# Optimization experiments

Measured on AMD Instinct MI355X. Metric: run time of the kernel, lower is better.

## Reference

```python
import jax, jax.numpy as jnp
import numpy as np

N, E, F, HID, HEADS, L, B, R = 50000, 400000, 64, 256, 4, 4, 16, 8
C = HID // HEADS  # per-head channels = 64
LN_EPS = 1e-5
NEG_SLOPE = 0.2  # GATConv LeakyReLU default


def _posenc(n, d):
    pos = jnp.arange(n, dtype=jnp.float32)[:, None]
    i = jnp.arange(d, dtype=jnp.float32)[None, :]
    rates = 1.0 / 10000.0 ** (2.0 * jnp.floor(i / 2.0) / d)
    ang = pos * rates
    return jnp.where(jnp.arange(d)[None, :] % 2 == 0, jnp.sin(ang), jnp.cos(ang))


def _layernorm(x, g, b):
    mu = x.mean(-1, keepdims=True)
    var = ((x - mu) ** 2).mean(-1, keepdims=True)
    return (x - mu) * jax.lax.rsqrt(var + LN_EPS) * g + b


def _gat_layer(x, src, dst, W, a_src, a_dst, bias):
    # x: [N, HID]; W: [HID, HID]; a_src/a_dst: [HEADS, C]; bias: [HID]
    h = (x @ W).reshape(N, HEADS, C)
    s_src = (h * a_src[None]).sum(-1)  # [N, HEADS]
    s_dst = (h * a_dst[None]).sum(-1)  # [N, HEADS]
    e = jax.nn.leaky_relu(s_src[src] + s_dst[dst], NEG_SLOPE)  # [E', HEADS]
    m = jax.ops.segment_max(e, dst, num_segments=N)
    ex = jnp.exp(e - m[dst])
    denom = jax.ops.segment_sum(ex, dst, num_segments=N)
    alpha = ex / denom[dst]  # softmax over incoming edges per dst node
    out = jax.ops.segment_sum(alpha[:, :, None] * h[src], dst, num_segments=N)
    return out.reshape(N, HID) + bias


def setup_inputs() -> dict:
    key = jax.random.key(0)
    ks = jax.random.split(key, 20)
    sc = 0.05
    batch = jnp.sort(jax.random.randint(ks[2], (N,), 0, B))
    return {
        "x": jax.random.normal(ks[0], (N, F), jnp.float32),
        "region_emb_w": jax.random.normal(ks[3], (R, F), jnp.float32) * sc,
        "in_proj_w": jax.random.normal(ks[4], (3 * F, HID), jnp.float32) * sc,
        "in_proj_b": jnp.zeros((HID,), jnp.float32),
        "gat_w": jax.random.normal(ks[5], (L, HID, HID), jnp.float32) * sc,
        "att_src": jax.random.normal(ks[6], (L, HEADS, C), jnp.float32) * sc,
        "att_dst": jax.random.normal(ks[7], (L, HEADS, C), jnp.float32) * sc,
        "gat_b": jnp.zeros((L, HID), jnp.float32),
        "ln_g": jnp.ones((L, HID), jnp.float32),
        "ln_b": jnp.zeros((L, HID), jnp.float32),
        "ro_w1": jax.random.normal(ks[8], (HID, HID), jnp.float32) * sc,
        "ro_b1": jnp.zeros((HID,), jnp.float32),
        "ro_w2": jax.random.normal(ks[9], (HID, HID), jnp.float32) * sc,
        "ro_b2": jnp.zeros((HID,), jnp.float32),
        "edge_index": jax.random.randint(ks[1], (2, E), 0, N),
        "batch": batch,
        "region_ids": jax.random.randint(ks[10], (N,), 0, R),
    }


def reference(x, region_emb_w, in_proj_w, in_proj_b, gat_w, att_src, att_dst,
              gat_b, ln_g, ln_b, ro_w1, ro_b1, ro_w2, ro_b2,
              edge_index, batch, region_ids):
    # input features: x | region embedding | sinusoidal posenc  -> [N, 3F]
    feats = jnp.concatenate([x, region_emb_w[region_ids], _posenc(N, F)], axis=-1)
    h = feats @ in_proj_w + in_proj_b
    # add self loops once (GATConv add_self_loops=True)
    loop = jnp.arange(N)
    src = jnp.concatenate([edge_index[0], loop])
    dst = jnp.concatenate([edge_index[1], loop])
    for l in range(L):
        h = _gat_layer(h, src, dst, gat_w[l], att_src[l], att_dst[l], gat_b[l])
        h = _layernorm(jax.nn.relu(h), ln_g[l], ln_b[l])
        # dropout is identity in eval mode
    # global mean pool over graphs
    sums = jax.ops.segment_sum(h, batch, num_segments=B)
    cnts = jax.ops.segment_sum(jnp.ones((N,), h.dtype), batch, num_segments=B)
    pooled = sums / jnp.maximum(cnts, 1.0)[:, None]  # [B, HID]
    out = jax.nn.gelu(pooled @ ro_w1 + ro_b1, approximate=False) @ ro_w2 + ro_b2
    return out
```

## Files before the change

kernel.cpp:

```cpp
#include <hip/hip_runtime.h>
#include <cmath>

typedef unsigned short u16;
typedef unsigned char u8;
typedef unsigned int u32;
typedef short bf16x8 __attribute__((ext_vector_type(8)));
typedef float f32x4 __attribute__((ext_vector_type(4)));
typedef float f32x2 __attribute__((ext_vector_type(2)));

#define NN 50000
#define MP 50048
#define EE 400000
#define ET 450000
#define HIDD 256
#define KIN 192
#define LN_EPSF 1e-5f

__device__ __forceinline__ float bf2f(u16 u){ return __uint_as_float(((u32)u)<<16); }
__device__ __forceinline__ u16 f2bf(float f){
  u32 x = __float_as_uint(f);
  u32 r = x + 0x7fffu + ((x>>16)&1u);
  return (u16)(r>>16);
}
__device__ __forceinline__ u32 pack2(float a, float b){ return (u32)f2bf(a) | ((u32)f2bf(b)<<16); }
__device__ __forceinline__ u8 f2fp8(float v){
  return (u8)(__builtin_amdgcn_cvt_pk_fp8_f32(v, v, 0, false) & 0xff);
}

__device__ __forceinline__ void dma16(const u16* g, u16* lds){
  __builtin_amdgcn_global_load_lds(
      (const __attribute__((address_space(1))) void*)g,
      (__attribute__((address_space(3))) void*)lds, 16, 0, 0);
}

__global__ __launch_bounds__(256) void k_setup(
    const float* __restrict__ x, const float* __restrict__ remb, const int* __restrict__ rid,
    u16* __restrict__ feats,
    const float* __restrict__ ipw, const float* __restrict__ gatw,
    u16* __restrict__ wtin, u16* __restrict__ wtl,
    const float* __restrict__ asrc, const float* __restrict__ adst, u16* __restrict__ vmat,
    const int* __restrict__ ei, int* __restrict__ deg)
{
  int b = blockIdx.x;
  if (b < 1564){
    int u = b*256 + threadIdx.x;
    int n = u >> 3;
    int c0 = (u & 7) * 8;
    uint4 o = {0u,0u,0u,0u};
    if (n < NN){
      const float* xp = x + (size_t)n*64 + c0;
      float4 v0 = *(const float4*)xp;
      float4 v1 = *(const float4*)(xp + 4);
      o.x = pack2(v0.x, v0.y); o.y = pack2(v0.z, v0.w);
      o.z = pack2(v1.x, v1.y); o.w = pack2(v1.z, v1.w);
    }
    *(uint4*)(feats + (size_t)n*192 + c0) = o;
  } else if (b < 3128){
    int u = (b-1564)*256 + threadIdx.x;
    int n = u >> 3;
    int c0 = (u & 7) * 8;
    uint4 o = {0u,0u,0u,0u};
    if (n < NN){
      const float* rp = remb + (size_t)rid[n]*64 + c0;
      float4 v0 = *(const float4*)rp;
      float4 v1 = *(const float4*)(rp + 4);
      o.x = pack2(v0.x, v0.y); o.y = pack2(v0.z, v0.w);
      o.z = pack2(v1.x, v1.y); o.w = pack2(v1.z, v1.w);
    }
    *(uint4*)(feats + (size_t)n*192 + 64 + c0) = o;
  } else if (b < 4692){
    int u = (b-3128)*256 + threadIdx.x;
    int n = u >> 3;
    int i0 = (u & 7) * 8;
    uint4 o = {0u,0u,0u,0u};
    if (n < NN){
      float fn = (float)n;
      float os[8];
      #pragma unroll
      for (int m=0;m<4;++m){
        float rate = exp2f(-(float)(i0 + 2*m) * (1.0f/64.0f) * 13.287712379549449f);
        float s, c;
        __sincosf(fn * rate, &s, &c);
        os[2*m] = s; os[2*m+1] = c;
      }
      o.x = pack2(os[0], os[1]); o.y = pack2(os[2], os[3]);
      o.z = pack2(os[4], os[5]); o.w = pack2(os[6], os[7]);
    }
    *(uint4*)(feats + (size_t)n*192 + 128 + i0) = o;
  } else if (b < 5908){
    int idx = (b - 4692)*256 + threadIdx.x;
    if (idx < 49152){
      int n = idx / 192, k = idx - n*192;
      wtin[idx] = f2bf(ipw[k*256 + n]);
    } else {
      int j = idx - 49152;
      if (j < 262144){
        int l = j >> 16, rem = j & 65535;
        int n = rem >> 8, k = rem & 255;
        wtl[j] = f2bf(gatw[l*65536 + k*256 + n]);
      }
    }
  } else if (b < 5972){
    int idx = (b - 5908)*256 + threadIdx.x;
    if (idx < 16384){
      int l = idx >> 12, rem = idx & 4095, v = rem >> 8, k = rem & 255;
      float s = 0.f;
      if (v < 8){
        const float* a = (v < 4) ? (asrc + l*256 + v*64) : (adst + l*256 + (v-4)*64);
        const float* w = gatw + (size_t)l*65536 + k*256 + (v & 3)*64;
        #pragma unroll 8
        for (int c=0;c<64;++c) s += w[c]*a[c];
      }
      vmat[idx] = f2bf(s);
    }
  } else {
    int i = (b - 5972)*256 + threadIdx.x;
    if (i < ET){
      int d = (i < EE) ? ei[EE + i] : (i - EE);
      atomicAdd(&deg[d], 1);
    }
  }
}

__global__ void k_scan1(const int* __restrict__ deg, int* __restrict__ row_off, int* __restrict__ part){
  __shared__ int s[256];
  int n = blockIdx.x*256 + threadIdx.x;
  int v = (n < NN) ? deg[n] : 0;
  s[threadIdx.x] = v;
  __syncthreads();
  for (int off=1; off<256; off<<=1){
    int t = (threadIdx.x >= off) ? s[threadIdx.x - off] : 0;
    __syncthreads();
    s[threadIdx.x] += t;
    __syncthreads();
  }
  if (n < NN) row_off[n] = s[threadIdx.x] - v;
  if (threadIdx.x == 255) part[blockIdx.x] = s[255];
}

__global__ void k_scan23(int* __restrict__ row_off, const int* __restrict__ part, int nparts){
  __shared__ int sp[256];
  int t = threadIdx.x;
  sp[t] = (t < nparts && t < (int)blockIdx.x) ? part[t] : 0;
  __syncthreads();
  for (int off=128; off; off>>=1){
    if (t < off) sp[t] += sp[t+off];
    __syncthreads();
  }
  int n = blockIdx.x*256 + t;
  if (n < NN) row_off[n] += sp[0];
}

__global__ void k_scatter(const int* __restrict__ ei, const int* __restrict__ row_off,
                          int* __restrict__ cur, int* __restrict__ csr_src){
  int i = blockIdx.x*blockDim.x + threadIdx.x;
  if (i >= ET) return;
  int s, d;
  if (i < EE){ s = ei[i]; d = ei[EE + i]; } else { s = i - EE; d = i - EE; }
  int pos = row_off[d] + atomicAdd(&cur[d], 1);
  csr_src[pos] = s;
}

template<int K>
__global__ __launch_bounds__(256, 3) void k_gemm(
    const u16* __restrict__ A, const u16* __restrict__ Wt,
    const float* __restrict__ bias, const u16* __restrict__ vmat,
    float* __restrict__ ss, float* __restrict__ sd,
    u16* __restrict__ C, u8* __restrict__ C8, int M)
{
  __shared__ u16 Asl[2][128*32];
  __shared__ u16 Bsl[2][128*32];
  int tid = threadIdx.x;
  int wave = tid >> 6, lane = tid & 63, quad = lane >> 4, lm = lane & 15;
  int r0 = blockIdx.x * 128;
  int cb = blockIdx.y;
  int rW = (wave >> 1) * 64;
  int cW = (wave & 1) * 64;
  bool doScore = vmat && (cb == 0) && ((wave & 1) == 0);

  f32x4 acc[4][4] = {};
  f32x4 accs[4] = {};

  auto stage = [&](int buf, int k0){
    for (int m = wave; m < 8; m += 4){
      int s = m*64 + lane;
      int r = s >> 2, p = s & 3;
      int c = p ^ ((r >> 2) & 3);
      dma16(A + (size_t)(r0 + r)*K + k0 + c*8, &Asl[buf][m*512]);
    }
    for (int m = wave; m < 8; m += 4){
      int s = m*64 + lane;
      int r = s >> 2, p = s & 3;
      int c = p ^ ((r >> 2) & 3);
      dma16(Wt + (size_t)(cb*128 + r)*K + k0 + c*8, &Bsl[buf][m*512]);
    }
  };

  stage(0, 0);
  __syncthreads();

  for (int ks = 0; ks < K/32; ++ks){
    int cur = ks & 1;
    if (ks + 1 < K/32) stage(cur ^ 1, (ks+1)*32);

    bf16x8 a[4], b[4];
    #pragma unroll
    for (int i=0;i<4;++i){
      int row = rW + i*16 + lm;
      int slot = row*4 + (quad ^ ((row >> 2) & 3));
      a[i] = *(const bf16x8*)(&Asl[cur][slot*8]);
    }
    #pragma unroll
    for (int j=0;j<4;++j){
      int row = cW + j*16 + lm;
      int slot = row*4 + (quad ^ ((row >> 2) & 3));
      b[j] = *(const bf16x8*)(&Bsl[cur][slot*8]);
    }
    #pragma unroll
    for (int i=0;i<4;++i)
      #pragma unroll
      for (int j=0;j<4;++j)
        acc[i][j] = __builtin_amdgcn_mfma_f32_16x16x32_bf16(a[i], b[j], acc[i][j], 0, 0, 0);
    if (doScore){
      bf16x8 bs = *(const bf16x8*)(vmat + (size_t)lm*K + ks*32 + quad*8);
      #pragma unroll
      for (int i=0;i<4;++i)
        accs[i] = __builtin_amdgcn_mfma_f32_16x16x32_bf16(a[i], bs, accs[i], 0, 0, 0);
    }
    __syncthreads();
  }

  if (doScore){
    #pragma unroll
    for (int i=0;i<4;++i){
      #pragma unroll
      for (int r=0;r<4;++r){
        int row = r0 + rW + i*16 + quad*4 + r;
        if (row < M){
          if (lm < 4)      ss[row*4 + lm]     = accs[i][r];
          else if (lm < 8) sd[row*4 + lm - 4] = accs[i][r];
        }
      }
    }
  }

  #pragma unroll
  for (int i=0;i<4;++i){
    #pragma unroll
    for (int r=0;r<4;++r){
      int row = r0 + rW + i*16 + quad*4 + r;
      if (row < M){
        #pragma unroll
        for (int j=0;j<4;++j){
          int col = cb*128 + cW + j*16 + lm;
          float v = acc[i][j][r];
          if (bias) v += bias[col];
          if (C)  C[(size_t)row*256 + col] = f2bf(v);
          if (C8) C8[(size_t)row*256 + col] = f2fp8(v);
        }
      }
    }
  }
}

__global__ __launch_bounds__(256) void k_aggregate(
    const u8* __restrict__ h8, const float* __restrict__ ssrc, const float* __restrict__ sdst,
    const int* __restrict__ row_off, const int* __restrict__ deg, const int* __restrict__ csr_src,
    const float* __restrict__ bias, const float* __restrict__ g, const float* __restrict__ bb,
    u16* __restrict__ hout, u8* __restrict__ hout8)
{
  int wv = (blockIdx.x*blockDim.x + threadIdx.x) >> 6;
  int lane = threadIdx.x & 63;
  int half = lane >> 5;
  int hl = lane & 31;
  int n = wv*2 + half;
  if (n >= NN) return;
  int c0 = hl*8;
  int head = hl >> 3;
  float sdh = sdst[n*4 + head];
  int ro = row_off[n];
  int dg = deg[n];
  float denA = 0.f, denB = 0.f;
  float a0=0,a1=0,a2=0,a3=0,a4=0,a5=0,a6=0,a7=0;
  float b0=0,b1=0,b2=0,b3=0,b4=0,b5=0,b6=0,b7=0;

  int sA = csr_src[ro];
  int sB = (1 < dg) ? csr_src[ro + 1] : 0;
  uint2 uA = *(const uint2*)(h8 + (size_t)sA*HIDD + c0);
  uint2 uB = *(const uint2*)(h8 + (size_t)sB*HIDD + c0);
  float fA = ssrc[sA*4 + head];
  float fB = ssrc[sB*4 + head];

  for (int j = 0; j < dg; j += 2){
    bool hasB = (j + 1 < dg);
    int nA = (j + 2 < dg) ? csr_src[ro + j + 2] : 0;
    int nB = (j + 3 < dg) ? csr_src[ro + j + 3] : 0;
    uint2 vA = *(const uint2*)(h8 + (size_t)nA*HIDD + c0);
    uint2 vB = *(const uint2*)(h8 + (size_t)nB*HIDD + c0);
    float gA = ssrc[nA*4 + head];
    float gB = ssrc[nB*4 + head];

    float eA = fA + sdh;
    eA = (eA > 0.f) ? eA : 0.2f*eA;
    float xA = __expf(eA);
    denA += xA;
    f32x2 pA0 = __builtin_amdgcn_cvt_pk_f32_fp8((int)uA.x, false);
    f32x2 pA1 = __builtin_amdgcn_cvt_pk_f32_fp8((int)uA.x, true);
    f32x2 pA2 = __builtin_amdgcn_cvt_pk_f32_fp8((int)uA.y, false);
    f32x2 pA3 = __builtin_amdgcn_cvt_pk_f32_fp8((int)uA.y, true);
    a0 += xA*pA0.x; a1 += xA*pA0.y; a2 += xA*pA1.x; a3 += xA*pA1.y;
    a4 += xA*pA2.x; a5 += xA*pA2.y; a6 += xA*pA3.x; a7 += xA*pA3.y;
    if (hasB){
      float eB = fB + sdh;
      eB = (eB > 0.f) ? eB : 0.2f*eB;
      float xB = __expf(eB);
      denB += xB;
      f32x2 pB0 = __builtin_amdgcn_cvt_pk_f32_fp8((int)uB.x, false);
      f32x2 pB1 = __builtin_amdgcn_cvt_pk_f32_fp8((int)uB.x, true);
      f32x2 pB2 = __builtin_amdgcn_cvt_pk_f32_fp8((int)uB.y, false);
      f32x2 pB3 = __builtin_amdgcn_cvt_pk_f32_fp8((int)uB.y, true);
      b0 += xB*pB0.x; b1 += xB*pB0.y; b2 += xB*pB1.x; b3 += xB*pB1.y;
      b4 += xB*pB2.x; b5 += xB*pB2.y; b6 += xB*pB3.x; b7 += xB*pB3.y;
    }
    sA = nA; sB = nB; uA = vA; uB = vB; fA = gA; fB = gB;
  }

  float inv = 1.f / (denA + denB);
  float y[8];
  y[0]=a0+b0; y[1]=a1+b1; y[2]=a2+b2; y[3]=a3+b3;
  y[4]=a4+b4; y[5]=a5+b5; y[6]=a6+b6; y[7]=a7+b7;
  float4 bi0 = *(const float4*)(bias + c0);
  float4 bi1 = *(const float4*)(bias + c0 + 4);
  y[0]=fmaxf(y[0]*inv+bi0.x,0.f); y[1]=fmaxf(y[1]*inv+bi0.y,0.f);
  y[2]=fmaxf(y[2]*inv+bi0.z,0.f); y[3]=fmaxf(y[3]*inv+bi0.w,0.f);
  y[4]=fmaxf(y[4]*inv+bi1.x,0.f); y[5]=fmaxf(y[5]*inv+bi1.y,0.f);
  y[6]=fmaxf(y[6]*inv+bi1.z,0.f); y[7]=fmaxf(y[7]*inv+bi1.w,0.f);
  float sum = (y[0]+y[1])+(y[2]+y[3])+((y[4]+y[5])+(y[6]+y[7]));
  #pragma unroll
  for (int o=16;o>=1;o>>=1) sum += __shfl_xor(sum, o);
  float mu = sum * (1.f/256.f);
  float d[8], sq = 0.f;
  #pragma unroll
  for (int k=0;k<8;++k){ d[k] = y[k]-mu; sq += d[k]*d[k]; }
  #pragma unroll
  for (int o=16;o>=1;o>>=1) sq += __shfl_xor(sq, o);
  float rs = rsqrtf(sq*(1.f/256.f) + LN_EPSF);
  float4 g0 = *(const float4*)(g + c0);
  float4 g1 = *(const float4*)(g + c0 + 4);
  float4 q0 = *(const float4*)(bb + c0);
  float4 q1 = *(const float4*)(bb + c0 + 4);
  float o0 = d[0]*rs*g0.x + q0.x, o1 = d[1]*rs*g0.y + q0.y;
  float o2 = d[2]*rs*g0.z + q0.z, o3 = d[3]*rs*g0.w + q0.w;
  float o4v= d[4]*rs*g1.x + q1.x, o5 = d[5]*rs*g1.y + q1.y;
  float o6 = d[6]*rs*g1.z + q1.z, o7 = d[7]*rs*g1.w + q1.w;
  if (hout8){
    u32 w0 = (u32)__builtin_amdgcn_cvt_pk_fp8_f32(o0, o1, 0, false);
    w0 = (u32)__builtin_amdgcn_cvt_pk_fp8_f32(o2, o3, (int)w0, true);
    u32 w1 = (u32)__builtin_amdgcn_cvt_pk_fp8_f32(o4v, o5, 0, false);
    w1 = (u32)__builtin_amdgcn_cvt_pk_fp8_f32(o6, o7, (int)w1, true);
    uint2 o8; o8.x = w0; o8.y = w1;
    *(uint2*)(hout8 + (size_t)n*HIDD + c0) = o8;
  } else {
    uint4 o4;
    o4.x = pack2(o0, o1);
    o4.y = pack2(o2, o3);
    o4.z = pack2(o4v, o5);
    o4.w = pack2(o6, o7);
    *(uint4*)(hout + (size_t)n*HIDD + c0) = o4;
  }
}

__global__ __launch_bounds__(256) void k_pool(
    const u8* __restrict__ h8, const int* __restrict__ batch,
    float* __restrict__ pooled, float* __restrict__ cnt)
{
  const int chunk = 50;
  int t = threadIdx.x;
  int n0 = blockIdx.x*chunk;
  int n1 = min(n0 + chunk, NN);
  if (n0 >= n1) return;
  float acc = 0.f;
  int curb = batch[n0];
  int runStart = n0;
  bool hi = (t & 2) != 0;
  for (int n=n0; n<n1; ++n){
    int b = batch[n];
    if (b != curb){
      atomicAdd(&pooled[curb*HIDD + t], acc);
      if (t == 0) atomicAdd(&cnt[curb], (float)(n - runStart));
      acc = 0.f; curb = b; runStart = n;
    }
    u32 w = *(const u32*)(h8 + (size_t)n*HIDD + (t & ~3));
    f32x2 p = hi ? __builtin_amdgcn_cvt_pk_f32_fp8((int)w, true)
                 : __builtin_amdgcn_cvt_pk_f32_fp8((int)w, false);
    acc += (t & 1) ? p.y : p.x;
  }
  atomicAdd(&pooled[curb*HIDD + t], acc);
  if (t == 0) atomicAdd(&cnt[curb], (float)(n1 - runStart));
}

__global__ __launch_bounds__(256) void k_readout(
    const float* __restrict__ pooled, const float* __restrict__ cnt,
    const float* __restrict__ w1, const float* __restrict__ b1,
    const float* __restrict__ w2, const float* __restrict__ b2,
    float* __restrict__ out)
{
  __shared__ float p[256], mid[256];
  int b = blockIdx.x, t = threadIdx.x;
  float c = fmaxf(cnt[b], 1.f);
  p[t] = pooled[b*HIDD + t] / c;
  __syncthreads();
  float acc = b1[t];
  for (int k=0;k<256;++k) acc += p[k]*w1[k*256+t];
  mid[t] = 0.5f*acc*(1.f + erff(acc*0.70710678118654752f));
  __syncthreads();
  float acc2 = b2[t];
  for (int k=0;k<256;++k) acc2 += mid[k]*w2[k*256+t];
  out[b*HIDD + t] = acc2;
}

extern "C" void kernel_launch(void* const* d_in, const int* in_sizes, int n_in,
                              void* d_out, int out_size, void* d_ws, size_t ws_size,
                              hipStream_t stream)
{
  const float* x    = (const float*)d_in[0];
  const float* remb = (const float*)d_in[1];
  const float* ipw  = (const float*)d_in[2];
  const float* ipb  = (const float*)d_in[3];
  const float* gatw = (const float*)d_in[4];
  const float* asrc = (const float*)d_in[5];
  const float* adst = (const float*)d_in[6];
  const float* gatb = (const float*)d_in[7];
  const float* lng  = (const float*)d_in[8];
  const float* lnb  = (const float*)d_in[9];
  const float* row1 = (const float*)d_in[10];
  const float* rob1 = (const float*)d_in[11];
  const float* row2 = (const float*)d_in[12];
  const float* rob2 = (const float*)d_in[13];
  const int* ei   = (const int*)d_in[14];
  const int* batch= (const int*)d_in[15];
  const int* rid  = (const int*)d_in[16];

  char* ws = (char*)d_ws;
  int*   deg  = (int*)  (ws + 0);
  int*   cur  = (int*)  (ws + 200192);
  float* cnt  = (float*)(ws + 400384);
  float* pool = (float*)(ws + 400640);
  int*   row  = (int*)  (ws + 417024);
  int*   part = (int*)  (ws + 617216);
  int*   csr  = (int*)  (ws + 618240);
  float* ss   = (float*)(ws + 2418432);
  float* sd   = (float*)(ws + 3219200);
  u16*   vmat = (u16*)  (ws + 4019968);
  u16*   feats= (u16*)  (ws + 4052736);
  u16*   wtin = (u16*)  (ws + 23271168);
  u16*   wtl  = (u16*)  (ws + 23369472);
  u16*   hA   = (u16*)  (ws + 23893760);
  u8*    hA8  = (u8*)   (ws + 23893760);
  u8*    hB8  = (u8*)   (ws + 49518336);

  (void)hipMemsetAsync(ws, 0, 417024, stream);

  k_setup <<<7730, 256, 0, stream>>>(x, remb, rid, feats, ipw, gatw, wtin, wtl,
                                     asrc, adst, vmat, ei, deg);
  k_scan1 <<<196, 256, 0, stream>>>(deg, row, part);
  k_scan23<<<196, 256, 0, stream>>>(row, part, 196);
  k_scatter<<<1758, 256, 0, stream>>>(ei, row, cur, csr);

  k_gemm<KIN><<<dim3(391,2), 256, 0, stream>>>(feats, wtin, ipb, nullptr,
                                               nullptr, nullptr, hA, nullptr, NN);

  for (int l = 0; l < 4; ++l){
    k_gemm<HIDD><<<dim3(391,2), 256, 0, stream>>>(hA, wtl + (size_t)l*HIDD*HIDD, nullptr,
                                                  vmat + (size_t)l*16*256, ss, sd,
                                                  nullptr, hB8, NN);
    if (l < 3){
      k_aggregate<<<6250, 256, 0, stream>>>(hB8, ss, sd, row, deg, csr,
                                            gatb + l*HIDD, lng + l*HIDD, lnb + l*HIDD,
                                            hA, nullptr);
    } else {
      k_aggregate<<<6250, 256, 0, stream>>>(hB8, ss, sd, row, deg, csr,
                                            gatb + l*HIDD, lng + l*HIDD, lnb + l*HIDD,
                                            nullptr, hA8);
    }
  }

  k_pool   <<<1000, 256, 0, stream>>>(hA8, batch, pool, cnt);
  k_readout<<<16, 256, 0, stream>>>(pool, cnt, row1, rob1, row2, rob2, (float*)d_out);
}
```

Before: 456.0 us.

## Fuse mean-pool into last aggregate and widen edge gather to four streams

Global mean pooling moves into the final aggregation kernel. Each block reduces its 8 LayerNorm'd node rows in shared memory and atomically adds into at most two batch segments. This removes the separate pool kernel and the fp8 write and re-read of the last hidden state. The per-node edge loop also becomes four independent accumulator chains with a two-step-ahead index prefetch, to hide more gather latency. The costs are more registers, which may lower occupancy, and a block-wide sync in the last layer. The pooling assumes each 8-node block spans at most two batch ids, which holds for sorted batches with many nodes per graph.

```diff
diff --git a/kernel.cpp b/kernel.cpp
--- a/kernel.cpp
+++ b/kernel.cpp
@@ -267,10 +267,14 @@
     const u8* __restrict__ h8, const float* __restrict__ ssrc, const float* __restrict__ sdst,
     const int* __restrict__ row_off, const int* __restrict__ deg, const int* __restrict__ csr_src,
     const float* __restrict__ bias, const float* __restrict__ g, const float* __restrict__ bb,
-    u16* __restrict__ hout, u8* __restrict__ hout8)
+    u16* __restrict__ hout,
+    const int* __restrict__ batch, float* __restrict__ pooled, float* __restrict__ cnt)
 {
-  int wv = (blockIdx.x*blockDim.x + threadIdx.x) >> 6;
-  int lane = threadIdx.x & 63;
+  __shared__ float psum[8][256];
+  __shared__ int   pb[8];
+  int tid = threadIdx.x;
+  int wv = (blockIdx.x*256 + tid) >> 6;
+  int lane = tid & 63;
   int half = lane >> 5;
   int hl = lane & 31;
   int n = wv*2 + half;
@@ -280,55 +284,56 @@
   float sdh = sdst[n*4 + head];
   int ro = row_off[n];
   int dg = deg[n];
-  float denA = 0.f, denB = 0.f;
-  float a0=0,a1=0,a2=0,a3=0,a4=0,a5=0,a6=0,a7=0;
-  float b0=0,b1=0,b2=0,b3=0,b4=0,b5=0,b6=0,b7=0;
-
-  int sA = csr_src[ro];
-  int sB = (1 < dg) ? csr_src[ro + 1] : 0;
-  uint2 uA = *(const uint2*)(h8 + (size_t)sA*HIDD + c0);
-  uint2 uB = *(const uint2*)(h8 + (size_t)sB*HIDD + c0);
-  float fA = ssrc[sA*4 + head];
-  float fB = ssrc[sB*4 + head];
-
-  for (int j = 0; j < dg; j += 2){
-    bool hasB = (j + 1 < dg);
-    int nA = (j + 2 < dg) ? csr_src[ro + j + 2] : 0;
-    int nB = (j + 3 < dg) ? csr_src[ro + j + 3] : 0;
-    uint2 vA = *(const uint2*)(h8 + (size_t)nA*HIDD + c0);
-    uint2 vB = *(const uint2*)(h8 + (size_t)nB*HIDD + c0);
-    float gA = ssrc[nA*4 + head];
-    float gB = ssrc[nB*4 + head];
-
-    float eA = fA + sdh;
-    eA = (eA > 0.f) ? eA : 0.2f*eA;
-    float xA = __expf(eA);
-    denA += xA;
-    f32x2 pA0 = __builtin_amdgcn_cvt_pk_f32_fp8((int)uA.x, false);
-    f32x2 pA1 = __builtin_amdgcn_cvt_pk_f32_fp8((int)uA.x, true);
-    f32x2 pA2 = __builtin_amdgcn_cvt_pk_f32_fp8((int)uA.y, false);
-    f32x2 pA3 = __builtin_amdgcn_cvt_pk_f32_fp8((int)uA.y, true);
-    a0 += xA*pA0.x; a1 += xA*pA0.y; a2 += xA*pA1.x; a3 += xA*pA1.y;
-    a4 += xA*pA2.x; a5 += xA*pA2.y; a6 += xA*pA3.x; a7 += xA*pA3.y;
-    if (hasB){
-      float eB = fB + sdh;
-      eB = (eB > 0.f) ? eB : 0.2f*eB;
-      float xB = __expf(eB);
-      denB += xB;
-      f32x2 pB0 = __builtin_amdgcn_cvt_pk_f32_fp8((int)uB.x, false);
-      f32x2 pB1 = __builtin_amdgcn_cvt_pk_f32_fp8((int)uB.x, true);
-      f32x2 pB2 = __builtin_amdgcn_cvt_pk_f32_fp8((int)uB.y, false);
-      f32x2 pB3 = __builtin_amdgcn_cvt_pk_f32_fp8((int)uB.y, true);
-      b0 += xB*pB0.x; b1 += xB*pB0.y; b2 += xB*pB1.x; b3 += xB*pB1.y;
-      b4 += xB*pB2.x; b5 += xB*pB2.y; b6 += xB*pB3.x; b7 += xB*pB3.y;
-    }
-    sA = nA; sB = nB; uA = vA; uB = vB; fA = gA; fB = gB;
-  }
-
-  float inv = 1.f / (denA + denB);
+  float den[4] = {0.f,0.f,0.f,0.f};
+  float ac[4][8] = {};
+
+  int s2[4]; uint2 u[4]; float f[4];
+  #pragma unroll
+  for (int c=0;c<4;++c){
+    int i0 = (c < dg) ? (ro + c) : ro;
+    int s = csr_src[i0];
+    u[c] = *(const uint2*)(h8 + (size_t)s*HIDD + c0);
+    f[c] = ssrc[s*4 + head];
+  }
+  #pragma unroll
+  for (int c=0;c<4;++c){
+    int i1 = (4 + c < dg) ? (ro + 4 + c) : ro;
+    s2[c] = csr_src[i1];
+  }
+
+  for (int j = 0; j < dg; j += 4){
+    uint2 nu[4]; float nf[4]; int ns[4];
+    #pragma unroll
+    for (int c=0;c<4;++c){
+      nu[c] = *(const uint2*)(h8 + (size_t)s2[c]*HIDD + c0);
+      nf[c] = ssrc[s2[c]*4 + head];
+    }
+    #pragma unroll
+    for (int c=0;c<4;++c){
+      int i2 = (j + 8 + c < dg) ? (ro + j + 8 + c) : ro;
+      ns[c] = csr_src[i2];
+    }
+    #pragma unroll
+    for (int c=0;c<4;++c){
+      float e = f[c] + sdh;
+      e = (e > 0.f) ? e : 0.2f*e;
+      float xv = (j + c < dg) ? __expf(e) : 0.f;
+      den[c] += xv;
+      f32x2 p0 = __builtin_amdgcn_cvt_pk_f32_fp8((int)u[c].x, false);
+      f32x2 p1 = __builtin_amdgcn_cvt_pk_f32_fp8((int)u[c].x, true);
+      f32x2 p2 = __builtin_amdgcn_cvt_pk_f32_fp8((int)u[c].y, false);
+      f32x2 p3 = __builtin_amdgcn_cvt_pk_f32_fp8((int)u[c].y, true);
+      ac[c][0] += xv*p0.x; ac[c][1] += xv*p0.y; ac[c][2] += xv*p1.x; ac[c][3] += xv*p1.y;
+      ac[c][4] += xv*p2.x; ac[c][5] += xv*p2.y; ac[c][6] += xv*p3.x; ac[c][7] += xv*p3.y;
+    }
+    #pragma unroll
+    for (int c=0;c<4;++c){ u[c]=nu[c]; f[c]=nf[c]; s2[c]=ns[c]; }
+  }
+
+  float inv = 1.f / ((den[0]+den[1])+(den[2]+den[3]));
   float y[8];
-  y[0]=a0+b0; y[1]=a1+b1; y[2]=a2+b2; y[3]=a3+b3;
-  y[4]=a4+b4; y[5]=a5+b5; y[6]=a6+b6; y[7]=a7+b7;
+  #pragma unroll
+  for (int k=0;k<8;++k) y[k] = (ac[0][k]+ac[1][k])+(ac[2][k]+ac[3][k]);
   float4 bi0 = *(const float4*)(bias + c0);
   float4 bi1 = *(const float4*)(bias + c0 + 4);
   y[0]=fmaxf(y[0]*inv+bi0.x,0.f); y[1]=fmaxf(y[1]*inv+bi0.y,0.f);
@@ -353,13 +358,29 @@
   float o2 = d[2]*rs*g0.z + q0.z, o3 = d[3]*rs*g0.w + q0.w;
   float o4v= d[4]*rs*g1.x + q1.x, o5 = d[5]*rs*g1.y + q1.y;
   float o6 = d[6]*rs*g1.z + q1.z, o7 = d[7]*rs*g1.w + q1.w;
-  if (hout8){
-    u32 w0 = (u32)__builtin_amdgcn_cvt_pk_fp8_f32(o0, o1, 0, false);
-    w0 = (u32)__builtin_amdgcn_cvt_pk_fp8_f32(o2, o3, (int)w0, true);
-    u32 w1 = (u32)__builtin_amdgcn_cvt_pk_fp8_f32(o4v, o5, 0, false);
-    w1 = (u32)__builtin_amdgcn_cvt_pk_fp8_f32(o6, o7, (int)w1, true);
-    uint2 o8; o8.x = w0; o8.y = w1;
-    *(uint2*)(hout8 + (size_t)n*HIDD + c0) = o8;
+
+  if (pooled){
+    int slot = tid >> 5;
+    *(float4*)&psum[slot][c0]     = make_float4(o0, o1, o2, o3);
+    *(float4*)&psum[slot][c0 + 4] = make_float4(o4v, o5, o6, o7);
+    if (hl == 0) pb[slot] = batch[n];
+    __syncthreads();
+    int b0 = pb[0], b7 = pb[7];
+    float sA = 0.f, sB = 0.f;
+    #pragma unroll
+    for (int s=0;s<8;++s){
+      float v = psum[s][tid];
+      if (pb[s] == b0) sA += v; else sB += v;
+    }
+    atomicAdd(&pooled[b0*HIDD + tid], sA);
+    if (b7 != b0) atomicAdd(&pooled[b7*HIDD + tid], sB);
+    if (tid == 0){
+      int cA = 0;
+      #pragma unroll
+      for (int s=0;s<8;++s) cA += (pb[s] == b0) ? 1 : 0;
+      atomicAdd(&cnt[b0], (float)cA);
+      if (b7 != b0) atomicAdd(&cnt[b7], (float)(8 - cA));
+    }
   } else {
     uint4 o4;
     o4.x = pack2(o0, o1);
@@ -368,35 +389,6 @@
     o4.w = pack2(o6, o7);
     *(uint4*)(hout + (size_t)n*HIDD + c0) = o4;
   }
-}
-
-__global__ __launch_bounds__(256) void k_pool(
-    const u8* __restrict__ h8, const int* __restrict__ batch,
-    float* __restrict__ pooled, float* __restrict__ cnt)
-{
-  const int chunk = 50;
-  int t = threadIdx.x;
-  int n0 = blockIdx.x*chunk;
-  int n1 = min(n0 + chunk, NN);
-  if (n0 >= n1) return;
-  float acc = 0.f;
-  int curb = batch[n0];
-  int runStart = n0;
-  bool hi = (t & 2) != 0;
-  for (int n=n0; n<n1; ++n){
-    int b = batch[n];
-    if (b != curb){
-      atomicAdd(&pooled[curb*HIDD + t], acc);
-      if (t == 0) atomicAdd(&cnt[curb], (float)(n - runStart));
-      acc = 0.f; curb = b; runStart = n;
-    }
-    u32 w = *(const u32*)(h8 + (size_t)n*HIDD + (t & ~3));
-    f32x2 p = hi ? __builtin_amdgcn_cvt_pk_f32_fp8((int)w, true)
-                 : __builtin_amdgcn_cvt_pk_f32_fp8((int)w, false);
-    acc += (t & 1) ? p.y : p.x;
-  }
-  atomicAdd(&pooled[curb*HIDD + t], acc);
-  if (t == 0) atomicAdd(&cnt[curb], (float)(n1 - runStart));
 }
 
 __global__ __launch_bounds__(256) void k_readout(
@@ -456,7 +448,6 @@
   u16*   wtin = (u16*)  (ws + 23271168);
   u16*   wtl  = (u16*)  (ws + 23369472);
   u16*   hA   = (u16*)  (ws + 23893760);
-  u8*    hA8  = (u8*)   (ws + 23893760);
   u8*    hB8  = (u8*)   (ws + 49518336);
 
   (void)hipMemsetAsync(ws, 0, 417024, stream);
@@ -477,14 +468,13 @@
     if (l < 3){
       k_aggregate<<<6250, 256, 0, stream>>>(hB8, ss, sd, row, deg, csr,
                                             gatb + l*HIDD, lng + l*HIDD, lnb + l*HIDD,
-                                            hA, nullptr);
+                                            hA, nullptr, nullptr, nullptr);
     } else {
       k_aggregate<<<6250, 256, 0, stream>>>(hB8, ss, sd, row, deg, csr,
                                             gatb + l*HIDD, lng + l*HIDD, lnb + l*HIDD,
-                                            nullptr, hA8);
-    }
-  }
-
-  k_pool   <<<1000, 256, 0, stream>>>(hA8, batch, pool, cnt);
+                                            nullptr, batch, pool, cnt);
+    }
+  }
+
   k_readout<<<16, 256, 0, stream>>>(pool, cnt, row1, rob1, row2, rob2, (float*)d_out);
 }
```

Measured after the change: 489.8 us. +7.4%, slower.

## Map one wavefront per node in aggregation with 4 channels per lane

Applied to the files above, without the earlier changes.

The GAT aggregation kernel changes from two nodes per 64-lane wavefront, each lane handling 8 fp8 channels, to one node per wavefront with each lane handling 4 channels. The grid doubles to match. The edge loop now prefetches CSR indices two iterations ahead and replaces the divergent hasB branch with a predicated zero weight. The goal is more parallelism and memory-level concurrency for the gather, and fewer registers per lane. In exchange, each gathered row is loaded as narrower 4-byte pieces, and per-node index and score loads are repeated across twice as many lanes.

```diff
diff --git a/kernel.cpp b/kernel.cpp
--- a/kernel.cpp
+++ b/kernel.cpp
@@ -269,104 +269,81 @@
     const float* __restrict__ bias, const float* __restrict__ g, const float* __restrict__ bb,
     u16* __restrict__ hout, u8* __restrict__ hout8)
 {
-  int wv = (blockIdx.x*blockDim.x + threadIdx.x) >> 6;
+  int n = (blockIdx.x*256 + threadIdx.x) >> 6;
   int lane = threadIdx.x & 63;
-  int half = lane >> 5;
-  int hl = lane & 31;
-  int n = wv*2 + half;
   if (n >= NN) return;
-  int c0 = hl*8;
-  int head = hl >> 3;
+  int c0 = lane*4;
+  int head = lane >> 4;
   float sdh = sdst[n*4 + head];
   int ro = row_off[n];
   int dg = deg[n];
   float denA = 0.f, denB = 0.f;
-  float a0=0,a1=0,a2=0,a3=0,a4=0,a5=0,a6=0,a7=0;
-  float b0=0,b1=0,b2=0,b3=0,b4=0,b5=0,b6=0,b7=0;
+  float a0=0,a1=0,a2=0,a3=0;
+  float b0=0,b1=0,b2=0,b3=0;
 
   int sA = csr_src[ro];
   int sB = (1 < dg) ? csr_src[ro + 1] : 0;
-  uint2 uA = *(const uint2*)(h8 + (size_t)sA*HIDD + c0);
-  uint2 uB = *(const uint2*)(h8 + (size_t)sB*HIDD + c0);
+  u32 uA = *(const u32*)(h8 + (size_t)sA*HIDD + c0);
+  u32 uB = *(const u32*)(h8 + (size_t)sB*HIDD + c0);
   float fA = ssrc[sA*4 + head];
   float fB = ssrc[sB*4 + head];
+  int pA = (2 < dg) ? csr_src[ro + 2] : 0;
+  int pB = (3 < dg) ? csr_src[ro + 3] : 0;
 
   for (int j = 0; j < dg; j += 2){
-    bool hasB = (j + 1 < dg);
-    int nA = (j + 2 < dg) ? csr_src[ro + j + 2] : 0;
-    int nB = (j + 3 < dg) ? csr_src[ro + j + 3] : 0;
-    uint2 vA = *(const uint2*)(h8 + (size_t)nA*HIDD + c0);
-    uint2 vB = *(const uint2*)(h8 + (size_t)nB*HIDD + c0);
-    float gA = ssrc[nA*4 + head];
-    float gB = ssrc[nB*4 + head];
+    u32 vA = *(const u32*)(h8 + (size_t)pA*HIDD + c0);
+    u32 vB = *(const u32*)(h8 + (size_t)pB*HIDD + c0);
+    float gA = ssrc[pA*4 + head];
+    float gB = ssrc[pB*4 + head];
+    int qA = (j + 4 < dg) ? csr_src[ro + j + 4] : 0;
+    int qB = (j + 5 < dg) ? csr_src[ro + j + 5] : 0;
 
     float eA = fA + sdh;
     eA = (eA > 0.f) ? eA : 0.2f*eA;
     float xA = __expf(eA);
     denA += xA;
-    f32x2 pA0 = __builtin_amdgcn_cvt_pk_f32_fp8((int)uA.x, false);
-    f32x2 pA1 = __builtin_amdgcn_cvt_pk_f32_fp8((int)uA.x, true);
-    f32x2 pA2 = __builtin_amdgcn_cvt_pk_f32_fp8((int)uA.y, false);
-    f32x2 pA3 = __builtin_amdgcn_cvt_pk_f32_fp8((int)uA.y, true);
+    f32x2 pA0 = __builtin_amdgcn_cvt_pk_f32_fp8((int)uA, false);
+    f32x2 pA1 = __builtin_amdgcn_cvt_pk_f32_fp8((int)uA, true);
     a0 += xA*pA0.x; a1 += xA*pA0.y; a2 += xA*pA1.x; a3 += xA*pA1.y;
-    a4 += xA*pA2.x; a5 += xA*pA2.y; a6 += xA*pA3.x; a7 += xA*pA3.y;
-    if (hasB){
-      float eB = fB + sdh;
-      eB = (eB > 0.f) ? eB : 0.2f*eB;
-      float xB = __expf(eB);
-      denB += xB;
-      f32x2 pB0 = __builtin_amdgcn_cvt_pk_f32_fp8((int)uB.x, false);
-      f32x2 pB1 = __builtin_amdgcn_cvt_pk_f32_fp8((int)uB.x, true);
-      f32x2 pB2 = __builtin_amdgcn_cvt_pk_f32_fp8((int)uB.y, false);
-      f32x2 pB3 = __builtin_amdgcn_cvt_pk_f32_fp8((int)uB.y, true);
-      b0 += xB*pB0.x; b1 += xB*pB0.y; b2 += xB*pB1.x; b3 += xB*pB1.y;
-      b4 += xB*pB2.x; b5 += xB*pB2.y; b6 += xB*pB3.x; b7 += xB*pB3.y;
-    }
-    sA = nA; sB = nB; uA = vA; uB = vB; fA = gA; fB = gB;
+
+    float eB = fB + sdh;
+    eB = (eB > 0.f) ? eB : 0.2f*eB;
+    float xB = (j + 1 < dg) ? __expf(eB) : 0.f;
+    denB += xB;
+    f32x2 pB0 = __builtin_amdgcn_cvt_pk_f32_fp8((int)uB, false);
+    f32x2 pB1 = __builtin_amdgcn_cvt_pk_f32_fp8((int)uB, true);
+    b0 += xB*pB0.x; b1 += xB*pB0.y; b2 += xB*pB1.x; b3 += xB*pB1.y;
+
+    uA = vA; uB = vB; fA = gA; fB = gB; pA = qA; pB = qB;
   }
 
   float inv = 1.f / (denA + denB);
-  float y[8];
-  y[0]=a0+b0; y[1]=a1+b1; y[2]=a2+b2; y[3]=a3+b3;
-  y[4]=a4+b4; y[5]=a5+b5; y[6]=a6+b6; y[7]=a7+b7;
-  float4 bi0 = *(const float4*)(bias + c0);
-  float4 bi1 = *(const float4*)(bias + c0 + 4);
-  y[0]=fmaxf(y[0]*inv+bi0.x,0.f); y[1]=fmaxf(y[1]*inv+bi0.y,0.f);
-  y[2]=fmaxf(y[2]*inv+bi0.z,0.f); y[3]=fmaxf(y[3]*inv+bi0.w,0.f);
-  y[4]=fmaxf(y[4]*inv+bi1.x,0.f); y[5]=fmaxf(y[5]*inv+bi1.y,0.f);
-  y[6]=fmaxf(y[6]*inv+bi1.z,0.f); y[7]=fmaxf(y[7]*inv+bi1.w,0.f);
-  float sum = (y[0]+y[1])+(y[2]+y[3])+((y[4]+y[5])+(y[6]+y[7]));
+  float y0 = (a0+b0)*inv, y1 = (a1+b1)*inv, y2 = (a2+b2)*inv, y3 = (a3+b3)*inv;
+  float4 bi = *(const float4*)(bias + c0);
+  y0 = fmaxf(y0 + bi.x, 0.f); y1 = fmaxf(y1 + bi.y, 0.f);
+  y2 = fmaxf(y2 + bi.z, 0.f); y3 = fmaxf(y3 + bi.w, 0.f);
+  float sum = (y0+y1)+(y2+y3);
   #pragma unroll
-  for (int o=16;o>=1;o>>=1) sum += __shfl_xor(sum, o);
+  for (int o=32;o>=1;o>>=1) sum += __shfl_xor(sum, o);
   float mu = sum * (1.f/256.f);
-  float d[8], sq = 0.f;
+  float d0 = y0-mu, d1 = y1-mu, d2 = y2-mu, d3 = y3-mu;
+  float sq = (d0*d0+d1*d1)+(d2*d2+d3*d3);
   #pragma unroll
-  for (int k=0;k<8;++k){ d[k] = y[k]-mu; sq += d[k]*d[k]; }
-  #pragma unroll
-  for (int o=16;o>=1;o>>=1) sq += __shfl_xor(sq, o);
+  for (int o=32;o>=1;o>>=1) sq += __shfl_xor(sq, o);
   float rs = rsqrtf(sq*(1.f/256.f) + LN_EPSF);
-  float4 g0 = *(const float4*)(g + c0);
-  float4 g1 = *(const float4*)(g + c0 + 4);
-  float4 q0 = *(const float4*)(bb + c0);
-  float4 q1 = *(const float4*)(bb + c0 + 4);
-  float o0 = d[0]*rs*g0.x + q0.x, o1 = d[1]*rs*g0.y + q0.y;
-  float o2 = d[2]*rs*g0.z + q0.z, o3 = d[3]*rs*g0.w + q0.w;
-  float o4v= d[4]*rs*g1.x + q1.x, o5 = d[5]*rs*g1.y + q1.y;
-  float o6 = d[6]*rs*g1.z + q1.z, o7 = d[7]*rs*g1.w + q1.w;
+  float4 gv = *(const float4*)(g + c0);
+  float4 qv = *(const float4*)(bb + c0);
+  float o0 = d0*rs*gv.x + qv.x, o1 = d1*rs*gv.y + qv.y;
+  float o2 = d2*rs*gv.z + qv.z, o3 = d3*rs*gv.w + qv.w;
   if (hout8){
     u32 w0 = (u32)__builtin_amdgcn_cvt_pk_fp8_f32(o0, o1, 0, false);
     w0 = (u32)__builtin_amdgcn_cvt_pk_fp8_f32(o2, o3, (int)w0, true);
-    u32 w1 = (u32)__builtin_amdgcn_cvt_pk_fp8_f32(o4v, o5, 0, false);
-    w1 = (u32)__builtin_amdgcn_cvt_pk_fp8_f32(o6, o7, (int)w1, true);
-    uint2 o8; o8.x = w0; o8.y = w1;
-    *(uint2*)(hout8 + (size_t)n*HIDD + c0) = o8;
+    *(u32*)(hout8 + (size_t)n*HIDD + c0) = w0;
   } else {
-    uint4 o4;
+    uint2 o4;
     o4.x = pack2(o0, o1);
     o4.y = pack2(o2, o3);
-    o4.z = pack2(o4v, o5);
-    o4.w = pack2(o6, o7);
-    *(uint4*)(hout + (size_t)n*HIDD + c0) = o4;
+    *(uint2*)(hout + (size_t)n*HIDD + c0) = o4;
   }
 }
 
@@ -475,13 +452,13 @@
                                                   vmat + (size_t)l*16*256, ss, sd,
                                                   nullptr, hB8, NN);
     if (l < 3){
-      k_aggregate<<<6250, 256, 0, stream>>>(hB8, ss, sd, row, deg, csr,
-                                            gatb + l*HIDD, lng + l*HIDD, lnb + l*HIDD,
-                                            hA, nullptr);
+      k_aggregate<<<12500, 256, 0, stream>>>(hB8, ss, sd, row, deg, csr,
+                                             gatb + l*HIDD, lng + l*HIDD, lnb + l*HIDD,
+                                             hA, nullptr);
     } else {
-      k_aggregate<<<6250, 256, 0, stream>>>(hB8, ss, sd, row, deg, csr,
-                                            gatb + l*HIDD, lng + l*HIDD, lnb + l*HIDD,
-                                            nullptr, hA8);
+      k_aggregate<<<12500, 256, 0, stream>>>(hB8, ss, sd, row, deg, csr,
+                                             gatb + l*HIDD, lng + l*HIDD, lnb + l*HIDD,
+                                             nullptr, hA8);
     }
   }
 
```

Result: slower. 468.7 us (+2.8%).
